# Kernel tuning notes

Hardware: AMD Instinct MI355X
Metric: run time of the kernel (lower is better)

The kernel has to match this reference:

```python
import jax, jax.numpy as jnp
import numpy as np
from itertools import combinations

UNSPOOL = np.array([h + b for h in combinations(range(0, 4), 2) for b in combinations(range(4, 9), 3)])  # (60,5)
EMB = 64

def _lrelu(v):
    return jax.nn.leaky_relu(v, 0.01)

def _unspool(x):
    # x: (M,18) int -> (1,M,60,5) ranks, suits
    x = x[None]
    ranks, suits = x[:, :, ::2], x[:, :, 1::2]
    hr, hs = ranks[:, :, :4], suits[:, :, :4]
    br, bs = ranks[:, :, 4:], suits[:, :, 4:]
    hi, bi = jnp.argsort(hs, -1), jnp.argsort(bs, -1)
    hr = jnp.take_along_axis(hr, hi, -1); hs = jnp.take_along_axis(hs, hi, -1)
    br = jnp.take_along_axis(br, bi, -1); bs = jnp.take_along_axis(bs, bi, -1)
    hi2, bi2 = jnp.argsort(hr, -1), jnp.argsort(br, -1)
    r = jnp.concatenate([jnp.take_along_axis(hr, hi2, -1), jnp.take_along_axis(br, bi2, -1)], -1)
    s = jnp.concatenate([jnp.take_along_axis(hs, hi2, -1), jnp.take_along_axis(bs, bi2, -1)], -1)
    return r[:, :, UNSPOOL], s[:, :, UNSPOOL]

def setup_inputs() -> dict:
    key = jax.random.key(0)
    ks = jax.random.split(key, 24)
    M, nA = 2048, 9
    ranks = jax.random.randint(ks[0], (M, 9), 1, 14)
    suits = jax.random.randint(ks[1], (M, 9), 1, 5)
    x = jnp.zeros((M, 18), jnp.int64 if jax.config.jax_enable_x64 else jnp.int32)
    x = x.at[:, ::2].set(ranks).at[:, 1::2].set(suits)
    def lin(k, i, o):
        kw, kb = jax.random.split(k)
        s = 1.0 / np.sqrt(i)
        return (jax.random.uniform(kw, (i, o), jnp.float32, -s, s),
                jax.random.uniform(kb, (o,), jnp.float32, -s, s))
    emb = jax.random.normal(ks[2], (53, EMB), jnp.float32)
    emb = emb.at[0].set(0.0)  # padding_idx=0
    hW1, hb1 = lin(ks[3], 128, 512); hW2, hb2 = lin(ks[4], 512, 128)
    bW1, bb1 = lin(ks[5], 192, 512); bW2, bb2 = lin(ks[6], 512, 128)
    oW1, ob1 = lin(ks[7], 15360, 512); oW2, ob2 = lin(ks[8], 512, 256); oW3, ob3 = lin(ks[9], 256, 127)
    sW, sb = lin(ks[10], 127, nA)
    return dict(x=x, emb=emb, hW1=hW1, hb1=hb1, hW2=hW2, hb2=hb2,
                bW1=bW1, bb1=bb1, bW2=bW2, bb2=bb2,
                oW1=oW1, ob1=ob1, oW2=oW2, ob2=ob2, oW3=oW3, ob3=ob3,
                sW=sW, sb=sb)

def reference(x, emb, hW1, hb1, hW2, hb2, bW1, bb1, bW2, bb2,
              oW1, ob1, oW2, ob2, oW3, ob3, sW, sb):
    M = x.shape[0]
    sr, ss = _unspool(x)                      # (1,M,60,5)
    cards = (sr - 1) * ss                     # 0..48, 0 is padding
    e = emb[cards]                            # (1,M,60,5,64)
    hero = e[..., :2, :].reshape(1, M, 60, 2 * EMB)    # (1,M,60,128)
    board = e[..., 2:, :].reshape(1, M, 60, 3 * EMB)   # (1,M,60,192)
    hero = _lrelu(_lrelu(hero @ hW1 + hb1) @ hW2 + hb2)
    board = _lrelu(_lrelu(board @ bW1 + bb1) @ bW2 + bb2)
    raw = jnp.concatenate([hero, board], -1).reshape(1, M, 60 * 256)  # (1,M,15360)
    r = _lrelu(raw @ oW1 + ob1)
    r = _lrelu(r @ oW2 + ob2)
    r = _lrelu(r @ oW3 + ob3)
    return r.reshape(M, -1) @ sW + sb         # (M,nA)
```

## Files before the change

### kernel.cpp

```cpp
#include <hip/hip_runtime.h>

typedef _Float16 f16;
typedef __attribute__((ext_vector_type(8))) _Float16 f16x8;
typedef __attribute__((ext_vector_type(4))) float f32x4;

__device__ inline float lrelu(float v){ return v > 0.f ? v : 0.01f*v; }
__device__ inline f16x8 lrelu8(f16x8 v){
    f16x8 z = {};
    f16x8 mx = __builtin_elementwise_max(v, z);
    f16x8 mn = __builtin_elementwise_min(v, z);
    return mx + mn * (f16)0.01f;
}

__device__ __forceinline__ void gload16(const void* gp, void* lp) {
    __builtin_amdgcn_global_load_lds(
        (const __attribute__((address_space(1))) unsigned int*)gp,
        (__attribute__((address_space(3))) unsigned int*)lp,
        16, 0, 0);
}

#define M_ROWS 2048

#define P1_T    0
#define P1_HW2  265
#define P1_BW2  393
#define P1_OW2  521
#define P1_OW3  777
#define P1_CARD 841
#define P1_END  845

__device__ void d_transpose512(const float* __restrict__ in, f16* __restrict__ out,
                               int K, int Nin, int Nout, int b, int tid) {
    int idx = b * 512 + tid;
    if (idx >= Nout * K) return;
    int n = idx / K, k = idx - n * K;
    float v = (n < Nin) ? in[(size_t)k * Nin + n] : 0.f;
    out[idx] = (f16)v;
}

__global__ __launch_bounds__(512) void prep1(const int* __restrict__ x,
                                             const float* __restrict__ emb,
                                             const float* __restrict__ hW1,
                                             const float* __restrict__ hb1,
                                             const float* __restrict__ hW2,
                                             const float* __restrict__ bW1,
                                             const float* __restrict__ bb1,
                                             const float* __restrict__ bW2,
                                             const float* __restrict__ oW2,
                                             const float* __restrict__ oW3,
                                             f16* __restrict__ T,
                                             f16* __restrict__ hW2t,
                                             f16* __restrict__ bW2t,
                                             f16* __restrict__ oW2t,
                                             f16* __restrict__ oW3t,
                                             int* __restrict__ cid) {
    const int bid = blockIdx.x, tid = threadIdx.x;
    if (bid < P1_HW2) {
        int b = bid;
        int slot = b / 53, card = b - slot * 53;
        const float* W = (slot < 2) ? (hW1 + slot * 64 * 512) : (bW1 + (slot - 2) * 64 * 512);
        const float* e = emb + card * 64;
        float acc = (slot == 1) ? hb1[tid] : ((slot == 4) ? bb1[tid] : 0.f);
        #pragma unroll 8
        for (int k = 0; k < 64; ++k) acc += e[k] * W[k * 512 + tid];
        T[(size_t)b * 512 + tid] = (f16)acc;
    } else if (bid < P1_BW2) {
        d_transpose512(hW2, hW2t, 512, 128, 128, bid - P1_HW2, tid);
    } else if (bid < P1_OW2) {
        d_transpose512(bW2, bW2t, 512, 128, 128, bid - P1_BW2, tid);
    } else if (bid < P1_OW3) {
        d_transpose512(oW2, oW2t, 512, 256, 256, bid - P1_OW2, tid);
    } else if (bid < P1_CARD) {
        d_transpose512(oW3, oW3t, 256, 127, 128, bid - P1_OW3, tid);
    } else {
        int m = (bid - P1_CARD) * 512 + tid;
        if (m >= M_ROWS) return;
        int kh[4], kb[5];
        #pragma unroll
        for (int i = 0; i < 4; ++i) { int r = x[m*18 + 2*i], s = x[m*18 + 2*i + 1]; kh[i] = r*8 + s; }
        #pragma unroll
        for (int i = 0; i < 5; ++i) { int r = x[m*18 + 8 + 2*i], s = x[m*18 + 9 + 2*i]; kb[i] = r*8 + s; }
        #pragma unroll
        for (int i = 1; i < 4; ++i) { int v = kh[i], j = i-1; while (j >= 0 && kh[j] > v) { kh[j+1]=kh[j]; --j; } kh[j+1]=v; }
        #pragma unroll
        for (int i = 1; i < 5; ++i) { int v = kb[i], j = i-1; while (j >= 0 && kb[j] > v) { kb[j+1]=kb[j]; --j; } kb[j+1]=v; }
        #pragma unroll
        for (int i = 0; i < 4; ++i) { int r = kh[i] >> 3, s = kh[i] & 7; cid[m*9 + i] = (r - 1) * s; }
        #pragma unroll
        for (int i = 0; i < 5; ++i) { int r = kb[i] >> 3, s = kb[i] & 7; cid[m*9 + 4 + i] = (r - 1) * s; }
    }
}

#define MG_L2  256
#define MG_END 768

__global__ __launch_bounds__(512) void mega(const int* __restrict__ cid,
                                            const f16* __restrict__ T,
                                            const f16* __restrict__ hW2t,
                                            const f16* __restrict__ bW2t,
                                            const float* __restrict__ hb2,
                                            const float* __restrict__ bb2,
                                            const float* __restrict__ oW1,
                                            f16* __restrict__ X,
                                            f16* __restrict__ Wct) {
    __shared__ __align__(16) char smem[51200];
    const int bid = blockIdx.x, tid = threadIdx.x;

    if (bid < MG_L2) {
        float (*tile)[65] = (float(*)[65])smem;
        int kb = bid & 31, nb = bid >> 5;
        int nl = tid & 63;
        for (int kl = tid >> 6; kl < 64; kl += 8) {
            int col = kb * 64 + kl;
            int p = col >> 7, r = col & 127;
            int n = nb * 64 + nl;
            float s = 0.f;
            if (p < 6) {
                #pragma unroll
                for (int j = 0; j < 10; ++j) s += oW1[(size_t)((p * 10 + j) * 256 + r) * 512 + n];
            } else {
                int t = p - 6;
                #pragma unroll
                for (int i = 0; i < 6; ++i) s += oW1[(size_t)((i * 10 + t) * 256 + 128 + r) * 512 + n];
            }
            tile[kl][nl] = s;
        }
        __syncthreads();
        for (int nl2 = tid >> 6; nl2 < 64; nl2 += 8) {
            int kl2 = tid & 63;
            Wct[(size_t)(nb * 64 + nl2) * 2048 + kb * 64 + kl2] = (f16)tile[kl2][nl2];
        }
        return;
    }

    f16 (*As)[64][72] = (f16(*)[64][72])smem;
    f16 (*Bs)[128*64] = (f16(*)[128*64])(smem + 18432);
    const int lbid = bid - MG_L2;
    const bool hero = lbid < 192;
    const int row0 = hero ? lbid * 64 : (lbid - 192) * 64;
    const f16* Bt = hero ? hW2t : bW2t;
    const float* bias = hero ? hb2 : bb2;
    const int lane = tid & 63, wave = tid >> 6;
    const int lr = lane & 15;
    const int rw = wave & 3, cw = wave >> 2;

    const int br = tid >> 3, c8 = (tid & 7) * 8;
    const int grow = row0 + br;
    const f16 *t0, *t1, *t2;
    if (hero) {
        const int HP0[6] = {0,0,0,1,1,2}, HP1[6] = {1,2,3,2,3,3};
        int m = grow / 6, p = grow - m * 6;
        t0 = T + (size_t)(0*53 + cid[m*9 + HP0[p]]) * 512;
        t1 = T + (size_t)(1*53 + cid[m*9 + HP1[p]]) * 512;
        t2 = T;
    } else {
        const int BT0[10] = {4,4,4,4,4,4,5,5,5,6};
        const int BT1[10] = {5,5,5,6,6,7,6,6,7,7};
        const int BT2[10] = {6,7,8,7,8,8,7,8,8,8};
        int m = grow / 10, t = grow - m * 10;
        t0 = T + (size_t)(2*53 + cid[m*9 + BT0[t]]) * 512;
        t1 = T + (size_t)(3*53 + cid[m*9 + BT1[t]]) * 512;
        t2 = T + (size_t)(4*53 + cid[m*9 + BT2[t]]) * 512;
    }

    auto stageB = [&](int buf, int k0) {
        #pragma unroll
        for (int i = 0; i < 2; ++i) {
            int c = tid + i * 512;
            int r = c >> 3, cc = c & 7;
            gload16(Bt + (size_t)r * 512 + k0 + ((cc ^ (r & 7)) << 3), (void*)&Bs[buf][c * 8]);
        }
    };
    auto buildA = [&](int buf, int k0) {
        f16x8 a = *(const f16x8*)(t0 + k0 + c8);
        f16x8 b = *(const f16x8*)(t1 + k0 + c8);
        f16x8 c = *(const f16x8*)(t2 + k0 + c8);
        *(f16x8*)&As[buf][br][c8] = lrelu8(a + b + c);
    };

    f32x4 acc[4] = {};
    stageB(0, 0); buildA(0, 0);
    __syncthreads();
    for (int t = 0; t < 8; ++t) {
        int cur = t & 1;
        if (t < 7) { stageB(cur ^ 1, (t + 1) * 64); buildA(cur ^ 1, (t + 1) * 64); }
        #pragma unroll
        for (int kk2 = 0; kk2 < 2; ++kk2) {
            int g  = kk2 * 4 + (lane >> 4);
            int eo = (g ^ (lr & 7)) << 3;
            f16x8 a = *(const f16x8*)&As[cur][rw*16 + lr][kk2*32 + (lane >> 4)*8];
            #pragma unroll
            for (int j = 0; j < 4; ++j) {
                f16x8 b = *(const f16x8*)&Bs[cur][(cw*64 + j*16 + lr)*64 + eo];
                acc[j] = __builtin_amdgcn_mfma_f32_16x16x32_f16(a, b, acc[j], 0, 0, 0);
            }
        }
        __syncthreads();
    }
    #pragma unroll
    for (int j = 0; j < 4; ++j)
    #pragma unroll
    for (int q = 0; q < 4; ++q) {
        int row = row0 + rw*16 + (lane >> 4)*4 + q;
        int col = cw*64 + j*16 + lr;
        float v = lrelu(acc[j][q] + bias[col]);
        size_t off;
        if (hero) { int m = row / 6,  p = row - m*6;  off = (size_t)m*2048 + p*128 + col; }
        else      { int m = row / 10, p = row - m*10; off = (size_t)m*2048 + 768 + p*128 + col; }
        X[off] = (f16)v;
    }
}

template<int BN>
__global__ __launch_bounds__(512) void gemm_f16(const f16* __restrict__ A,
                                                const f16* __restrict__ Bt,
                                                const float* __restrict__ bias,
                                                f16* __restrict__ C,
                                                int K_, int ldc) {
    __shared__ __align__(16) f16 As[2][64 * 64];
    __shared__ __align__(16) f16 Bs[2][BN * 64];
    const int row0 = blockIdx.x * 64, col0 = blockIdx.y * BN;
    const int tid = threadIdx.x, lane = tid & 63, wave = tid >> 6;
    const int rw = wave >> 1, cw = wave & 1;
    const int lr = lane & 15;
    constexpr int NF = BN / 32;

    auto stage = [&](int buf, int k0) {
        { int c = tid; int r = c >> 3, cc = c & 7;
          gload16(A + (size_t)(row0 + r) * K_ + k0 + ((cc ^ (r & 7)) << 3), (void*)&As[buf][c * 8]); }
        for (int c = tid; c < BN * 8; c += 512) {
          int r = c >> 3, cc = c & 7;
          gload16(Bt + (size_t)(col0 + r) * K_ + k0 + ((cc ^ (r & 7)) << 3), (void*)&Bs[buf][c * 8]); }
    };

    f32x4 acc[NF] = {};
    stage(0, 0);
    __syncthreads();
    const int nt = K_ >> 6;
    for (int t = 0; t < nt; ++t) {
        int cur = t & 1;
        if (t + 1 < nt) stage(cur ^ 1, (t + 1) * 64);
        #pragma unroll
        for (int kk2 = 0; kk2 < 2; ++kk2) {
            int g  = kk2 * 4 + (lane >> 4);
            int eo = (g ^ (lr & 7)) << 3;
            f16x8 a = *(const f16x8*)&As[cur][(rw*16 + lr)*64 + eo];
            #pragma unroll
            for (int j = 0; j < NF; ++j) {
                f16x8 b = *(const f16x8*)&Bs[cur][(cw*(BN/2) + j*16 + lr)*64 + eo];
                acc[j] = __builtin_amdgcn_mfma_f32_16x16x32_f16(a, b, acc[j], 0, 0, 0);
            }
        }
        __syncthreads();
    }
    #pragma unroll
    for (int j = 0; j < NF; ++j)
    #pragma unroll
    for (int q = 0; q < 4; ++q) {
        int row = row0 + rw*16 + (lane >> 4)*4 + q;
        int col = col0 + cw*(BN/2) + j*16 + lr;
        C[(size_t)row * ldc + col] = (f16)lrelu(acc[j][q] + bias[col]);
    }
}

__global__ __launch_bounds__(256) void tail_kernel(const f16* __restrict__ R2,
                                                   const f16* __restrict__ oW3t,
                                                   const float* __restrict__ ob3,
                                                   const float* __restrict__ sW,
                                                   const float* __restrict__ sb,
                                                   float* __restrict__ out) {
    __shared__ __align__(16) f16 As[16 * 256];
    __shared__ __align__(16) f16 Bs[128 * 256];
    __shared__ float R3s[16][132];
    __shared__ float sWs[127 * 9];
    __shared__ float sbs[9];
    const int row0 = blockIdx.x * 16;
    const int tid = threadIdx.x, lane = tid & 63, wave = tid >> 6;
    const int lr = lane & 15;

    for (int c = tid; c < 512; c += 256) {
        int r = c >> 5, cc = c & 31;
        gload16(R2 + (size_t)(row0 + r) * 256 + ((cc ^ (r & 7)) << 3), (void*)&As[c * 8]);
    }
    for (int c = tid; c < 4096; c += 256) {
        int r = c >> 5, cc = c & 31;
        gload16(oW3t + (size_t)r * 256 + ((cc ^ (r & 7)) << 3), (void*)&Bs[c * 8]);
    }
    for (int i = tid; i < 127 * 9; i += 256) sWs[i] = sW[i];
    if (tid < 9) sbs[tid] = sb[tid];
    __syncthreads();

    f32x4 acc[2] = {};
    #pragma unroll
    for (int kk2 = 0; kk2 < 8; ++kk2) {
        int g  = kk2 * 4 + (lane >> 4);
        int eo = (g ^ (lr & 7)) << 3;
        f16x8 a = *(const f16x8*)&As[lr * 256 + eo];
        #pragma unroll
        for (int j = 0; j < 2; ++j) {
            f16x8 b = *(const f16x8*)&Bs[(wave*32 + j*16 + lr) * 256 + eo];
            acc[j] = __builtin_amdgcn_mfma_f32_16x16x32_f16(a, b, acc[j], 0, 0, 0);
        }
    }
    #pragma unroll
    for (int j = 0; j < 2; ++j)
    #pragma unroll
    for (int q = 0; q < 4; ++q) {
        int row = (lane >> 4)*4 + q;
        int col = wave*32 + j*16 + lr;
        float b = (col < 127) ? ob3[col] : 0.f;
        R3s[row][col] = lrelu(acc[j][q] + b);
    }
    __syncthreads();
    if (tid < 16 * 9) {
        int row = tid / 9, a = tid - row * 9;
        float s = sbs[a];
        #pragma unroll 4
        for (int n = 0; n < 127; ++n) s += R3s[row][n] * sWs[n * 9 + a];
        out[(size_t)(row0 + row) * 9 + a] = s;
    }
}

extern "C" void kernel_launch(void* const* d_in, const int* in_sizes, int n_in,
                              void* d_out, int out_size, void* d_ws, size_t ws_size,
                              hipStream_t stream) {
    const int*   x    = (const int*)  d_in[0];
    const float* emb  = (const float*)d_in[1];
    const float* hW1  = (const float*)d_in[2];
    const float* hb1  = (const float*)d_in[3];
    const float* hW2  = (const float*)d_in[4];
    const float* hb2  = (const float*)d_in[5];
    const float* bW1  = (const float*)d_in[6];
    const float* bb1  = (const float*)d_in[7];
    const float* bW2  = (const float*)d_in[8];
    const float* bb2  = (const float*)d_in[9];
    const float* oW1  = (const float*)d_in[10];
    const float* ob1  = (const float*)d_in[11];
    const float* oW2  = (const float*)d_in[12];
    const float* ob2  = (const float*)d_in[13];
    const float* oW3  = (const float*)d_in[14];
    const float* ob3  = (const float*)d_in[15];
    const float* sW   = (const float*)d_in[16];
    const float* sb   = (const float*)d_in[17];

    char* ws = (char*)d_ws;
    constexpr size_t OFF_T    = 0;
    constexpr size_t OFF_HW2T = 271360;
    constexpr size_t OFF_BW2T = OFF_HW2T + 131072;
    constexpr size_t OFF_OW2T = OFF_BW2T + 131072;
    constexpr size_t OFF_OW3T = OFF_OW2T + 262144;
    constexpr size_t OFF_WCT  = OFF_OW3T + 65536;
    constexpr size_t OFF_CID  = OFF_WCT + 2097152;
    constexpr size_t OFF_X    = OFF_CID + 73728;
    constexpr size_t OFF_R1   = OFF_X + 8388608;
    constexpr size_t OFF_R2   = OFF_R1 + 2097152;

    f16*  T    = (f16*)(ws + OFF_T);
    f16*  hW2t = (f16*)(ws + OFF_HW2T);
    f16*  bW2t = (f16*)(ws + OFF_BW2T);
    f16*  oW2t = (f16*)(ws + OFF_OW2T);
    f16*  oW3t = (f16*)(ws + OFF_OW3T);
    f16*  Wct  = (f16*)(ws + OFF_WCT);
    int*  cid  = (int*)(ws + OFF_CID);
    f16*  X    = (f16*)(ws + OFF_X);
    f16*  R1   = (f16*)(ws + OFF_R1);
    f16*  R2   = (f16*)(ws + OFF_R2);

    prep1<<<P1_END, 512, 0, stream>>>(x, emb, hW1, hb1, hW2, bW1, bb1, bW2,
                                      oW2, oW3, T, hW2t, bW2t, oW2t, oW3t, cid);
    mega<<<MG_END, 512, 0, stream>>>(cid, T, hW2t, bW2t, hb2, bb2, oW1, X, Wct);
    gemm_f16<64><<<dim3(32, 8), 512, 0, stream>>>(X,  Wct,  ob1, R1, 2048, 512);
    gemm_f16<32><<<dim3(32, 8), 512, 0, stream>>>(R1, oW2t, ob2, R2, 512, 256);
    tail_kernel<<<128, 256, 0, stream>>>(R2, oW3t, ob3, sW, sb, (float*)d_out);
}
```

Before: 60.53 us.

## Split-K the big GEMM, fuse layer-2/3 and head into one tail kernel

The oW2/oW3 weight transposes move from prep1 into the mega kernel. The K=2048 GEMM becomes a 2-way split-K combine kernel with 128-wide N tiles and an XCD-aware block mapping, writing fp32 partials. A new tail2 kernel sums the partials, applies bias and leaky ReLU, then runs the 512->256 and 256->127 GEMMs and the final head in one block per 16 rows. This removes one launch and the R1/R2 round trips, at the cost of fp32 partial traffic and less parallelism in the fused tail.

```diff
diff --git a/kernel.cpp b/kernel.cpp
--- a/kernel.cpp
+++ b/kernel.cpp
@@ -2,6 +2,7 @@
 
 typedef _Float16 f16;
 typedef __attribute__((ext_vector_type(8))) _Float16 f16x8;
+typedef __attribute__((ext_vector_type(4))) _Float16 f16x4;
 typedef __attribute__((ext_vector_type(4))) float f32x4;
 
 __device__ inline float lrelu(float v){ return v > 0.f ? v : 0.01f*v; }
@@ -24,10 +25,8 @@
 #define P1_T    0
 #define P1_HW2  265
 #define P1_BW2  393
-#define P1_OW2  521
-#define P1_OW3  777
-#define P1_CARD 841
-#define P1_END  845
+#define P1_CARD 521
+#define P1_END  525
 
 __device__ void d_transpose512(const float* __restrict__ in, f16* __restrict__ out,
                                int K, int Nin, int Nout, int b, int tid) {
@@ -46,13 +45,9 @@
                                              const float* __restrict__ bW1,
                                              const float* __restrict__ bb1,
                                              const float* __restrict__ bW2,
-                                             const float* __restrict__ oW2,
-                                             const float* __restrict__ oW3,
                                              f16* __restrict__ T,
                                              f16* __restrict__ hW2t,
                                              f16* __restrict__ bW2t,
-                                             f16* __restrict__ oW2t,
-                                             f16* __restrict__ oW3t,
                                              int* __restrict__ cid) {
     const int bid = blockIdx.x, tid = threadIdx.x;
     if (bid < P1_HW2) {
@@ -66,12 +61,8 @@
         T[(size_t)b * 512 + tid] = (f16)acc;
     } else if (bid < P1_BW2) {
         d_transpose512(hW2, hW2t, 512, 128, 128, bid - P1_HW2, tid);
-    } else if (bid < P1_OW2) {
+    } else if (bid < P1_CARD) {
         d_transpose512(bW2, bW2t, 512, 128, 128, bid - P1_BW2, tid);
-    } else if (bid < P1_OW3) {
-        d_transpose512(oW2, oW2t, 512, 256, 256, bid - P1_OW2, tid);
-    } else if (bid < P1_CARD) {
-        d_transpose512(oW3, oW3t, 256, 127, 128, bid - P1_OW3, tid);
     } else {
         int m = (bid - P1_CARD) * 512 + tid;
         if (m >= M_ROWS) return;
@@ -91,18 +82,24 @@
     }
 }
 
-#define MG_L2  256
-#define MG_END 768
-
-__global__ __launch_bounds__(512) void mega(const int* __restrict__ cid,
-                                            const f16* __restrict__ T,
-                                            const f16* __restrict__ hW2t,
-                                            const f16* __restrict__ bW2t,
-                                            const float* __restrict__ hb2,
-                                            const float* __restrict__ bb2,
-                                            const float* __restrict__ oW1,
-                                            f16* __restrict__ X,
-                                            f16* __restrict__ Wct) {
+#define MG_L2   256
+#define MG_OW2  768
+#define MG_OW3  1024
+#define MG_END  1088
+
+__global__ __launch_bounds__(512, 4) void mega(const int* __restrict__ cid,
+                                               const f16* __restrict__ T,
+                                               const f16* __restrict__ hW2t,
+                                               const f16* __restrict__ bW2t,
+                                               const float* __restrict__ hb2,
+                                               const float* __restrict__ bb2,
+                                               const float* __restrict__ oW1,
+                                               const float* __restrict__ oW2,
+                                               const float* __restrict__ oW3,
+                                               f16* __restrict__ X,
+                                               f16* __restrict__ Wct,
+                                               f16* __restrict__ oW2t,
+                                               f16* __restrict__ oW3t) {
     __shared__ __align__(16) char smem[51200];
     const int bid = blockIdx.x, tid = threadIdx.x;
 
@@ -132,6 +129,14 @@
         }
         return;
     }
+    if (bid >= MG_OW3) {
+        d_transpose512(oW3, oW3t, 256, 127, 128, bid - MG_OW3, tid);
+        return;
+    }
+    if (bid >= MG_OW2) {
+        d_transpose512(oW2, oW2t, 512, 256, 256, bid - MG_OW2, tid);
+        return;
+    }
 
     f16 (*As)[64][72] = (f16(*)[64][72])smem;
     f16 (*Bs)[128*64] = (f16(*)[128*64])(smem + 18432);
@@ -211,66 +216,74 @@
     }
 }
 
-template<int BN>
-__global__ __launch_bounds__(512) void gemm_f16(const f16* __restrict__ A,
-                                                const f16* __restrict__ Bt,
-                                                const float* __restrict__ bias,
-                                                f16* __restrict__ C,
-                                                int K_, int ldc) {
+__global__ __launch_bounds__(512, 4) void combine(const f16* __restrict__ X,
+                                                  const f16* __restrict__ Wct,
+                                                  float* __restrict__ R1p) {
     __shared__ __align__(16) f16 As[2][64 * 64];
-    __shared__ __align__(16) f16 Bs[2][BN * 64];
-    const int row0 = blockIdx.x * 64, col0 = blockIdx.y * BN;
+    __shared__ __align__(16) f16 Bs[2][128 * 64];
+    const int bid = blockIdx.x;
+    const int xcd = bid & 7, slot = bid >> 3;
+    const int rp = xcd * 4 + (slot & 3);
+    const int rest = slot >> 2;
+    const int cp = rest & 3, ks = rest >> 2;
+    const int row0 = rp * 64, col0 = cp * 128, k0b = ks * 1024;
     const int tid = threadIdx.x, lane = tid & 63, wave = tid >> 6;
-    const int rw = wave >> 1, cw = wave & 1;
+    const int rw = wave & 3, cw = wave >> 2;
     const int lr = lane & 15;
-    constexpr int NF = BN / 32;
 
     auto stage = [&](int buf, int k0) {
-        { int c = tid; int r = c >> 3, cc = c & 7;
-          gload16(A + (size_t)(row0 + r) * K_ + k0 + ((cc ^ (r & 7)) << 3), (void*)&As[buf][c * 8]); }
-        for (int c = tid; c < BN * 8; c += 512) {
-          int r = c >> 3, cc = c & 7;
-          gload16(Bt + (size_t)(col0 + r) * K_ + k0 + ((cc ^ (r & 7)) << 3), (void*)&Bs[buf][c * 8]); }
+        { int r = tid >> 3, cc = tid & 7;
+          gload16(X + (size_t)(row0 + r) * 2048 + k0 + ((cc ^ (r & 7)) << 3), (void*)&As[buf][tid * 8]); }
+        #pragma unroll
+        for (int i = 0; i < 2; ++i) {
+            int c = tid + i * 512;
+            int r = c >> 3, cc = c & 7;
+            gload16(Wct + (size_t)(col0 + r) * 2048 + k0 + ((cc ^ (r & 7)) << 3), (void*)&Bs[buf][c * 8]);
+        }
     };
 
-    f32x4 acc[NF] = {};
-    stage(0, 0);
+    f32x4 acc[4] = {};
+    stage(0, k0b);
     __syncthreads();
-    const int nt = K_ >> 6;
-    for (int t = 0; t < nt; ++t) {
+    for (int t = 0; t < 16; ++t) {
         int cur = t & 1;
-        if (t + 1 < nt) stage(cur ^ 1, (t + 1) * 64);
+        if (t < 15) stage(cur ^ 1, k0b + (t + 1) * 64);
         #pragma unroll
         for (int kk2 = 0; kk2 < 2; ++kk2) {
             int g  = kk2 * 4 + (lane >> 4);
             int eo = (g ^ (lr & 7)) << 3;
-            f16x8 a = *(const f16x8*)&As[cur][(rw*16 + lr)*64 + eo];
+            f16x8 a = *(const f16x8*)&As[cur][(rw * 16 + lr) * 64 + eo];
             #pragma unroll
-            for (int j = 0; j < NF; ++j) {
-                f16x8 b = *(const f16x8*)&Bs[cur][(cw*(BN/2) + j*16 + lr)*64 + eo];
+            for (int j = 0; j < 4; ++j) {
+                f16x8 b = *(const f16x8*)&Bs[cur][(cw * 64 + j * 16 + lr) * 64 + eo];
                 acc[j] = __builtin_amdgcn_mfma_f32_16x16x32_f16(a, b, acc[j], 0, 0, 0);
             }
         }
         __syncthreads();
     }
-    #pragma unroll
-    for (int j = 0; j < NF; ++j)
+    float* dst = R1p + (size_t)ks * 2048 * 512;
+    #pragma unroll
+    for (int j = 0; j < 4; ++j)
     #pragma unroll
     for (int q = 0; q < 4; ++q) {
-        int row = row0 + rw*16 + (lane >> 4)*4 + q;
-        int col = col0 + cw*(BN/2) + j*16 + lr;
-        C[(size_t)row * ldc + col] = (f16)lrelu(acc[j][q] + bias[col]);
-    }
-}
-
-__global__ __launch_bounds__(256) void tail_kernel(const f16* __restrict__ R2,
-                                                   const f16* __restrict__ oW3t,
-                                                   const float* __restrict__ ob3,
-                                                   const float* __restrict__ sW,
-                                                   const float* __restrict__ sb,
-                                                   float* __restrict__ out) {
-    __shared__ __align__(16) f16 As[16 * 256];
-    __shared__ __align__(16) f16 Bs[128 * 256];
+        int row = row0 + rw * 16 + (lane >> 4) * 4 + q;
+        int col = col0 + cw * 64 + j * 16 + lr;
+        dst[(size_t)row * 512 + col] = acc[j][q];
+    }
+}
+
+__global__ __launch_bounds__(512, 2) void tail2(const float* __restrict__ R1p,
+                                                const float* __restrict__ ob1,
+                                                const f16* __restrict__ oW2t,
+                                                const float* __restrict__ ob2,
+                                                const f16* __restrict__ oW3t,
+                                                const float* __restrict__ ob3,
+                                                const float* __restrict__ sW,
+                                                const float* __restrict__ sb,
+                                                float* __restrict__ out) {
+    __shared__ __align__(16) f16 A1s[16 * 512];
+    __shared__ __align__(16) f16 Bs[2][256 * 64];
+    __shared__ __align__(16) f16 R2s[16 * 256];
     __shared__ float R3s[16][132];
     __shared__ float sWs[127 * 9];
     __shared__ float sbs[9];
@@ -278,40 +291,97 @@
     const int tid = threadIdx.x, lane = tid & 63, wave = tid >> 6;
     const int lr = lane & 15;
 
-    for (int c = tid; c < 512; c += 256) {
-        int r = c >> 5, cc = c & 31;
-        gload16(R2 + (size_t)(row0 + r) * 256 + ((cc ^ (r & 7)) << 3), (void*)&As[c * 8]);
-    }
-    for (int c = tid; c < 4096; c += 256) {
-        int r = c >> 5, cc = c & 31;
-        gload16(oW3t + (size_t)r * 256 + ((cc ^ (r & 7)) << 3), (void*)&Bs[c * 8]);
-    }
-    for (int i = tid; i < 127 * 9; i += 256) sWs[i] = sW[i];
+    auto stageB2 = [&](int buf, int t) {
+        #pragma unroll
+        for (int i = 0; i < 4; ++i) {
+            int c = tid + i * 512;
+            int r = c >> 3, cc = c & 7;
+            gload16(oW2t + (size_t)r * 512 + t * 64 + ((cc ^ (r & 7)) << 3), (void*)&Bs[buf][c * 8]);
+        }
+    };
+    stageB2(0, 0);
+
+    #pragma unroll
+    for (int i = 0; i < 4; ++i) {
+        int g = tid + i * 512;
+        int row = g >> 7, c4 = (g & 127) << 2;
+        f32x4 a = *(const f32x4*)(R1p + (size_t)(row0 + row) * 512 + c4);
+        f32x4 b = *(const f32x4*)(R1p + (size_t)2048 * 512 + (size_t)(row0 + row) * 512 + c4);
+        f32x4 o = *(const f32x4*)(ob1 + c4);
+        f16x4 p;
+        #pragma unroll
+        for (int q = 0; q < 4; ++q) p[q] = (f16)lrelu(a[q] + b[q] + o[q]);
+        int chunk = c4 >> 3, half = (c4 >> 2) & 1;
+        *(f16x4*)&A1s[row * 512 + ((chunk ^ (row & 7)) << 3) + half * 4] = p;
+    }
+    for (int i = tid; i < 127 * 9; i += 512) sWs[i] = sW[i];
     if (tid < 9) sbs[tid] = sb[tid];
     __syncthreads();
 
-    f32x4 acc[2] = {};
-    #pragma unroll
-    for (int kk2 = 0; kk2 < 8; ++kk2) {
-        int g  = kk2 * 4 + (lane >> 4);
-        int eo = (g ^ (lr & 7)) << 3;
-        f16x8 a = *(const f16x8*)&As[lr * 256 + eo];
-        #pragma unroll
-        for (int j = 0; j < 2; ++j) {
-            f16x8 b = *(const f16x8*)&Bs[(wave*32 + j*16 + lr) * 256 + eo];
-            acc[j] = __builtin_amdgcn_mfma_f32_16x16x32_f16(a, b, acc[j], 0, 0, 0);
-        }
+    f32x4 acc2[2] = {};
+    for (int t = 0; t < 8; ++t) {
+        int cur = t & 1;
+        if (t < 7) stageB2(cur ^ 1, t + 1);
+        #pragma unroll
+        for (int kk2 = 0; kk2 < 2; ++kk2) {
+            int g  = kk2 * 4 + (lane >> 4);
+            int gg = t * 8 + g;
+            f16x8 a = *(const f16x8*)&A1s[lr * 512 + ((gg ^ (lr & 7)) << 3)];
+            int eo = (g ^ (lr & 7)) << 3;
+            #pragma unroll
+            for (int j = 0; j < 2; ++j) {
+                f16x8 b = *(const f16x8*)&Bs[cur][(wave * 32 + j * 16 + lr) * 64 + eo];
+                acc2[j] = __builtin_amdgcn_mfma_f32_16x16x32_f16(a, b, acc2[j], 0, 0, 0);
+            }
+        }
+        __syncthreads();
     }
     #pragma unroll
     for (int j = 0; j < 2; ++j)
     #pragma unroll
     for (int q = 0; q < 4; ++q) {
-        int row = (lane >> 4)*4 + q;
-        int col = wave*32 + j*16 + lr;
-        float b = (col < 127) ? ob3[col] : 0.f;
-        R3s[row][col] = lrelu(acc[j][q] + b);
-    }
+        int row = (lane >> 4) * 4 + q;
+        int col = wave * 32 + j * 16 + lr;
+        f16 v = (f16)lrelu(acc2[j][q] + ob2[col]);
+        int chunk = col >> 3, w = col & 7;
+        R2s[row * 256 + ((chunk ^ (row & 7)) << 3) + w] = v;
+    }
+    auto stageB3 = [&](int buf, int t) {
+        #pragma unroll
+        for (int i = 0; i < 2; ++i) {
+            int c = tid + i * 512;
+            if (c < 1024) {
+                int r = c >> 3, cc = c & 7;
+                gload16(oW3t + (size_t)r * 256 + t * 64 + ((cc ^ (r & 7)) << 3), (void*)&Bs[buf][c * 8]);
+            }
+        }
+    };
+    stageB3(0, 0);
     __syncthreads();
+
+    f32x4 acc3 = {};
+    for (int t = 0; t < 4; ++t) {
+        int cur = t & 1;
+        if (t < 3) stageB3(cur ^ 1, t + 1);
+        #pragma unroll
+        for (int kk2 = 0; kk2 < 2; ++kk2) {
+            int g  = kk2 * 4 + (lane >> 4);
+            int gg = t * 8 + g;
+            f16x8 a = *(const f16x8*)&R2s[lr * 256 + ((gg ^ (lr & 7)) << 3)];
+            int eo = (g ^ (lr & 7)) << 3;
+            f16x8 b = *(const f16x8*)&Bs[cur][(wave * 16 + lr) * 64 + eo];
+            acc3 = __builtin_amdgcn_mfma_f32_16x16x32_f16(a, b, acc3, 0, 0, 0);
+        }
+        __syncthreads();
+    }
+    #pragma unroll
+    for (int q = 0; q < 4; ++q) {
+        int row = (lane >> 4) * 4 + q;
+        int col = wave * 16 + lr;
+        R3s[row][col] = lrelu(acc3[q] + ((col < 127) ? ob3[col] : 0.f));
+    }
+    __syncthreads();
+
     if (tid < 16 * 9) {
         int row = tid / 9, a = tid - row * 9;
         float s = sbs[a];
@@ -352,24 +422,22 @@
     constexpr size_t OFF_WCT  = OFF_OW3T + 65536;
     constexpr size_t OFF_CID  = OFF_WCT + 2097152;
     constexpr size_t OFF_X    = OFF_CID + 73728;
-    constexpr size_t OFF_R1   = OFF_X + 8388608;
-    constexpr size_t OFF_R2   = OFF_R1 + 2097152;
-
-    f16*  T    = (f16*)(ws + OFF_T);
-    f16*  hW2t = (f16*)(ws + OFF_HW2T);
-    f16*  bW2t = (f16*)(ws + OFF_BW2T);
-    f16*  oW2t = (f16*)(ws + OFF_OW2T);
-    f16*  oW3t = (f16*)(ws + OFF_OW3T);
-    f16*  Wct  = (f16*)(ws + OFF_WCT);
-    int*  cid  = (int*)(ws + OFF_CID);
-    f16*  X    = (f16*)(ws + OFF_X);
-    f16*  R1   = (f16*)(ws + OFF_R1);
-    f16*  R2   = (f16*)(ws + OFF_R2);
+    constexpr size_t OFF_R1P  = OFF_X + 8388608;
+
+    f16*   T    = (f16*)(ws + OFF_T);
+    f16*   hW2t = (f16*)(ws + OFF_HW2T);
+    f16*   bW2t = (f16*)(ws + OFF_BW2T);
+    f16*   oW2t = (f16*)(ws + OFF_OW2T);
+    f16*   oW3t = (f16*)(ws + OFF_OW3T);
+    f16*   Wct  = (f16*)(ws + OFF_WCT);
+    int*   cid  = (int*)(ws + OFF_CID);
+    f16*   X    = (f16*)(ws + OFF_X);
+    float* R1p  = (float*)(ws + OFF_R1P);
 
     prep1<<<P1_END, 512, 0, stream>>>(x, emb, hW1, hb1, hW2, bW1, bb1, bW2,
-                                      oW2, oW3, T, hW2t, bW2t, oW2t, oW3t, cid);
-    mega<<<MG_END, 512, 0, stream>>>(cid, T, hW2t, bW2t, hb2, bb2, oW1, X, Wct);
-    gemm_f16<64><<<dim3(32, 8), 512, 0, stream>>>(X,  Wct,  ob1, R1, 2048, 512);
-    gemm_f16<32><<<dim3(32, 8), 512, 0, stream>>>(R1, oW2t, ob2, R2, 512, 256);
-    tail_kernel<<<128, 256, 0, stream>>>(R2, oW3t, ob3, sW, sb, (float*)d_out);
-}
+                                      T, hW2t, bW2t, cid);
+    mega<<<MG_END, 512, 0, stream>>>(cid, T, hW2t, bW2t, hb2, bb2,
+                                     oW1, oW2, oW3, X, Wct, oW2t, oW3t);
+    combine<<<256, 512, 0, stream>>>(X, Wct, R1p);
+    tail2<<<128, 512, 0, stream>>>(R1p, ob1, oW2t, ob2, oW3t, ob3, sW, sb, (float*)d_out);
+}
```

After: 56.21 us. 7.1% less time.
